# Kernel tuning notes

Measured on AMD Instinct MI355X. Metric: run time of the kernel, lower is better.

## Reference

```python
import jax, jax.numpy as jnp
import numpy as np

COST_CLASS, COST_BBOX, COST_GIOU = 1.0, 5.0, 2.0


def _lsa(cost):
    """Rectangular linear sum assignment (minimize), Jonker-Volgenant style.
    Returns (row_ind, col_ind) like scipy.optimize.linear_sum_assignment."""
    c = np.asarray(cost, dtype=np.float64)
    transposed = c.shape[0] > c.shape[1]
    if transposed:
        c = c.T
    n, m = c.shape  # n <= m
    INF = 1e18
    u = np.zeros(n + 1)
    v = np.zeros(m + 1)
    p = np.zeros(m + 1, dtype=np.int64)   # p[j]: row (1-based) matched to col j, 0 = free
    way = np.zeros(m + 1, dtype=np.int64)
    for i in range(1, n + 1):
        p[0] = i
        j0 = 0
        minv = np.full(m + 1, INF)
        used = np.zeros(m + 1, dtype=bool)
        while True:
            used[j0] = True
            i0 = p[j0]
            cur = c[i0 - 1, :] - u[i0] - v[1:]
            mv = minv[1:]
            upd = (~used[1:]) & (cur < mv)
            mv[upd] = cur[upd]
            way[1:][upd] = j0
            masked = np.where(used[1:], INF, mv)
            j1 = int(np.argmin(masked)) + 1
            delta = masked[j1 - 1]
            u[p[used]] += delta
            v[used] -= delta
            minv[1:][~used[1:]] -= delta
            j0 = j1
            if p[j0] == 0:
                break
        while j0:
            j1 = way[j0]
            p[j0] = p[j1]
            j0 = j1
    rows = p[1:] - 1
    cols = np.arange(m)
    keep = rows >= 0
    ri, ci = rows[keep], cols[keep]
    if transposed:
        ri, ci = ci, ri
    order = np.argsort(ri)
    return ri[order], ci[order]


def _solve_blocks(cost, n_per):
    """cost: np [Q, B*n_per]; solve LSA per diagonal block, return 0/1 solution."""
    Q, T = cost.shape
    B = T // n_per
    sol = np.zeros((Q, T), dtype=np.float32)
    for b in range(B):
        ri, ci = _lsa(cost[:, b * n_per:(b + 1) * n_per])
        sol[ri, b * n_per + ci] = 1.0
    return sol


def box_cxcywh_to_xyxy(b):
    cx, cy, w, h = jnp.split(b, 4, axis=-1)
    return jnp.concatenate([cx - 0.5 * w, cy - 0.5 * h, cx + 0.5 * w, cy + 0.5 * h], axis=-1)


def generalized_box_iou(b1, b2):
    # b1: [N,4] xyxy, b2: [M,4] xyxy -> [N,M]
    area1 = (b1[:, 2] - b1[:, 0]) * (b1[:, 3] - b1[:, 1])
    area2 = (b2[:, 2] - b2[:, 0]) * (b2[:, 3] - b2[:, 1])
    lt = jnp.maximum(b1[:, None, :2], b2[None, :, :2])
    rb = jnp.minimum(b1[:, None, 2:], b2[None, :, 2:])
    wh = jnp.clip(rb - lt, 0.0)
    inter = wh[..., 0] * wh[..., 1]
    union = area1[:, None] + area2[None, :] - inter
    iou = inter / union
    ltc = jnp.minimum(b1[:, None, :2], b2[None, :, :2])
    rbc = jnp.maximum(b1[:, None, 2:], b2[None, :, 2:])
    whc = jnp.clip(rbc - ltc, 0.0)
    areac = whc[..., 0] * whc[..., 1]
    return iou - (areac - union) / areac


def build_cost(pred_logits, pred_boxes, tgt_labels, tgt_boxes, n_per):
    B, Q, C = pred_logits.shape
    out_prob = jax.nn.softmax(pred_logits.reshape(B * Q, C), axis=-1)
    out_bbox = pred_boxes.reshape(B * Q, 4)
    cost_class = -out_prob[:, tgt_labels]                                  # [N,T]
    cost_bbox = jnp.sum(jnp.abs(out_bbox[:, None, :] - tgt_boxes[None, :, :]), axis=-1)  # L1 cdist
    cost_giou = -generalized_box_iou(box_cxcywh_to_xyxy(out_bbox), box_cxcywh_to_xyxy(tgt_boxes))
    cm = COST_BBOX * cost_bbox + COST_CLASS * cost_class + COST_GIOU * cost_giou
    cm = cm.reshape(B, Q, B, n_per)
    blocks = cm[jnp.arange(B), :, jnp.arange(B), :]        # diagonal blocks [B,Q,n_per]
    return jnp.transpose(blocks, (1, 0, 2)).reshape(Q, B * n_per)  # hstack -> [Q, T]


def setup_inputs() -> dict:
    key = jax.random.key(0)
    k1, k2, k3, k4 = jax.random.split(key, 4)
    B, Q, C, n_per = 16, 900, 92, 32
    T = B * n_per
    return {
        "pred_logits": jax.random.normal(k1, (B, Q, C), dtype=jnp.float32),
        "pred_boxes": jax.random.uniform(k2, (B, Q, 4), dtype=jnp.float32),
        "tgt_labels": jax.random.randint(k3, (T,), 0, C, dtype=jnp.int64),
        "tgt_boxes": jax.random.uniform(k4, (T, 4), dtype=jnp.float32),
        "n_targets": n_per,
    }


def reference(pred_logits, pred_boxes, tgt_labels, tgt_boxes, n_targets):
    n_per = int(n_targets)
    cost = build_cost(pred_logits, pred_boxes, tgt_labels, tgt_boxes, n_per)
    sol = jax.pure_callback(
        lambda c: _solve_blocks(np.asarray(c, dtype=np.float64), n_per),
        jax.ShapeDtypeStruct(cost.shape, jnp.float32),
        cost,
    )
    return sol
```

## Files before the change

kernel.cpp:

```cpp
#include <hip/hip_runtime.h>
#include <math.h>

#define BB 16
#define QQ 900
#define CC 92
#define NP 32
#define TT (BB*NP)
#define RSTRIDE 1024
#define NT 512

#define WSC_COST 0
#define WSC_MAX  (BB*NP*RSTRIDE*4)
#define WSC_SUM  (WSC_MAX + BB*QQ*4)
#define WSC_A    (WSC_SUM + BB*QQ*4)
#define WS_NEED  (WSC_A + TT*4)

__device__ __forceinline__ double mkdbl(int lo, int hi) {
    return __longlong_as_double(((long long)hi << 32) | (unsigned int)lo);
}
__device__ __forceinline__ double readlane_dbl(double x, int s) {
    long long l = __double_as_longlong(x);
    int lo = __builtin_amdgcn_readlane((int)l, s);
    int hi = __builtin_amdgcn_readlane((int)(l >> 32), s);
    return mkdbl(lo, hi);
}

#define DPP_MIN64(CTRL)                                                       \
    {                                                                         \
        long long _l = __double_as_longlong(m);                               \
        int _lo = (int)_l, _hi = (int)(_l >> 32);                             \
        int _olo = __builtin_amdgcn_update_dpp(_lo, _lo, CTRL, 0xf, 0xf, false); \
        int _ohi = __builtin_amdgcn_update_dpp(_hi, _hi, CTRL, 0xf, 0xf, false); \
        m = fmin(m, mkdbl(_olo, _ohi));                                       \
    }

__launch_bounds__(256)
__global__ void denom_kernel(const float* __restrict__ logits,
                             float* __restrict__ wmax,
                             float* __restrict__ wsum)
{
    int idx = blockIdx.x * 256 + threadIdx.x;
    if (idx >= BB * QQ) return;
    const float4* row4 = (const float4*)(logits + (size_t)idx * CC);
    float mx = -INFINITY;
    #pragma unroll
    for (int k = 0; k < 23; ++k) {
        float4 x = row4[k];
        mx = fmaxf(mx, x.x); mx = fmaxf(mx, x.y);
        mx = fmaxf(mx, x.z); mx = fmaxf(mx, x.w);
    }
    float s = 0.f;
    #pragma unroll
    for (int k = 0; k < 23; ++k) {
        float4 x = row4[k];
        s += expf(x.x - mx); s += expf(x.y - mx);
        s += expf(x.z - mx); s += expf(x.w - mx);
    }
    wmax[idx] = mx;
    wsum[idx] = s;
}

__launch_bounds__(256)
__global__ void cost_kernel(const float* __restrict__ logits,
                            const float* __restrict__ pboxes,
                            const int*   __restrict__ labels,
                            const float* __restrict__ tboxes,
                            const float* __restrict__ wmax,
                            const float* __restrict__ wsum,
                            float* __restrict__ wcost)
{
    const int r = blockIdx.x;
    const int b = r >> 5, t = r & 31;
    const float* lg = logits + (size_t)b * QQ * CC;
    const float* pb = pboxes + (size_t)b * QQ * 4;
    const float* tb = tboxes + (size_t)b * NP * 4;
    const float* smax = wmax + b * QQ;
    const float* ssum = wsum + b * QQ;

    const float t0 = tb[t*4+0], t1 = tb[t*4+1], t2 = tb[t*4+2], t3 = tb[t*4+3];
    const int   lt = labels[b * NP + t];
    const float tx1 = t0 - 0.5f*t2, ty1 = t1 - 0.5f*t3;
    const float tx2 = t0 + 0.5f*t2, ty2 = t1 + 0.5f*t3;
    const float area2 = (tx2-tx1)*(ty2-ty1);

    float* crow = wcost + (size_t)r * RSTRIDE;
    for (int q = threadIdx.x; q < RSTRIDE; q += 256) {
        float val = 0.f;
        if (q < QQ) {
            float l    = lg[q * CC + lt];
            float prob = expf(l - smax[q]) / ssum[q];
            float cclass = -prob;
            float p0 = pb[q*4+0], p1 = pb[q*4+1], p2 = pb[q*4+2], p3 = pb[q*4+3];
            float cbbox = fabsf(p0-t0) + fabsf(p1-t1)
                        + fabsf(p2-t2) + fabsf(p3-t3);
            float px1 = p0 - 0.5f*p2, py1 = p1 - 0.5f*p3;
            float px2 = p0 + 0.5f*p2, py2 = p1 + 0.5f*p3;
            float area1 = (px2-px1)*(py2-py1);
            float ltx = fmaxf(px1,tx1), lty = fmaxf(py1,ty1);
            float rbx = fminf(px2,tx2), rby = fminf(py2,ty2);
            float wx = fmaxf(rbx-ltx, 0.f), wy = fmaxf(rby-lty, 0.f);
            float inter = wx*wy;
            float uni = area1 + area2 - inter;
            float iou = inter / uni;
            float cx1 = fminf(px1,tx1), cy1 = fminf(py1,ty1);
            float cx2 = fmaxf(px2,tx2), cy2 = fmaxf(py2,ty2);
            float cwx = fmaxf(cx2-cx1, 0.f), cwy = fmaxf(cy2-cy1, 0.f);
            float areac = cwx*cwy;
            float giou = iou - (areac - uni) / areac;
            val = 5.f*cbbox + 1.f*cclass + 2.f*(-giou);
        }
        crow[q] = val;
    }
}

#define C_OFF_COST 0
#define C_SZ_COST  (NP * RSTRIDE * 4)
#define C_OFF_U    (C_OFF_COST + C_SZ_COST)
#define C_OFF_V    (C_OFF_U + 264)
#define C_OFF_FLAG (C_OFF_V + 7208)
#define C_DYN      (C_OFF_FLAG + 128)

__launch_bounds__(256)
__global__ void walk_kernel(const float* __restrict__ wcost,
                            int* __restrict__ wa)
{
    extern __shared__ char smem[];
    float*  s_cost = (float*)(smem + C_OFF_COST);
    double* s_u    = (double*)(smem + C_OFF_U);
    double* s_v    = (double*)(smem + C_OFF_V);
    volatile int* s_flag = (volatile int*)(smem + C_OFF_FLAG);

    const int b    = blockIdx.x;
    const int tid  = threadIdx.x;
    const int wv   = tid >> 6;
    const int lane = tid & 63;

    if (tid < 32) s_flag[tid] = 0;
    __syncthreads();

    if (wv != 0) {
        for (int t = wv - 1; t < NP; t += 3) {
            const float4* src =
                (const float4*)(wcost + ((size_t)(b * NP + t) * RSTRIDE));
            float4* dst = (float4*)(s_cost + t * RSTRIDE);
            float4 v0 = src[lane];
            float4 v1 = src[lane + 64];
            float4 v2 = src[lane + 128];
            float4 v3 = src[lane + 192];
            dst[lane]       = v0;
            dst[lane + 64]  = v1;
            dst[lane + 128] = v2;
            dst[lane + 192] = v3;
            asm volatile("s_waitcnt vmcnt(0) lgkmcnt(0)" ::: "memory");
            if (lane == 0) s_flag[t] = 1;
        }
        return;
    }

    for (int j = lane; j <= QQ; j += 64) s_v[j] = 0.0;
    if (lane <= NP) s_u[lane] = 0.0;
    asm volatile("s_waitcnt lgkmcnt(0)" ::: "memory");

    int acol = 0;
    const float4* cbase4 = (const float4*)s_cost;

    double vreg[16];
    #pragma unroll
    for (int k = 0; k < 16; ++k) {
        int col = 4 * lane + ((k >> 2) << 8) + (k & 3) + 1;
        vreg[k] = (col <= QQ) ? 0.0 : -1.0e300;
    }

    int nv = 0;

    while (nv < 1) {
        if (s_flag[0]) nv = 1;
        else __builtin_amdgcn_s_sleep(2);
    }
    float4 cf[4];
    {
        const float4* crow4 = cbase4;
        #pragma unroll
        for (int k = 0; k < 4; ++k) cf[k] = crow4[lane + (k << 6)];
    }

    for (int i = 1; i <= NP; ++i) {
        int i0 = i, j1prev = 0, T = 0;
        int path_reg = 1, row_reg = 1;

        for (int t = 1;; ++t) {
            if (lane == t) row_reg = i0;
            if (j1prev) {
                #pragma unroll
                for (int k = 0; k < 16; ++k) {
                    int col = 4 * lane + ((k >> 2) << 8) + (k & 3) + 1;
                    if (col == j1prev) vreg[k] = -1.0e300;
                }
            }

            double key[16];
            #pragma unroll
            for (int k = 0; k < 4; ++k) {
                const float* cp = (const float*)&cf[k];
                #pragma unroll
                for (int e2 = 0; e2 < 4; ++e2) {
                    int kk  = 4 * k + e2;
                    int col = 4 * lane + (k << 8) + e2 + 1;
                    double d = (double)cp[e2] - vreg[kk];
                    long long bits =
                        (__double_as_longlong(d) & ~2047LL) | (long long)col;
                    key[kk] = __longlong_as_double(bits);
                }
            }
            double a0 = fmin(key[0], key[1]),   a1 = fmin(key[2], key[3]);
            double a2 = fmin(key[4], key[5]),   a3 = fmin(key[6], key[7]);
            double a4 = fmin(key[8], key[9]),   a5 = fmin(key[10], key[11]);
            double a6 = fmin(key[12], key[13]), a7 = fmin(key[14], key[15]);
            double b0 = fmin(a0, a1), b1 = fmin(a2, a3);
            double b2 = fmin(a4, a5), b3 = fmin(a6, a7);
            double m  = fmin(fmin(b0, b1), fmin(b2, b3));

            DPP_MIN64(0x111);
            DPP_MIN64(0x112);
            DPP_MIN64(0x114);
            DPP_MIN64(0x118);
            DPP_MIN64(0x142);
            DPP_MIN64(0x143);

            int wlo = __builtin_amdgcn_readlane((int)__double_as_longlong(m), 63);
            int j1  = wlo & 2047;

            if (lane == t) path_reg = j1;

            unsigned long long mask = __ballot(acol == j1);
            if (mask == 0) { T = t; break; }
            int L = (int)__builtin_ctzll(mask);
            i0 = L + 1;
            j1prev = j1;

            const float4* crow4 = cbase4 + (size_t)L * (RSTRIDE / 4);
            #pragma unroll
            for (int k = 0; k < 4; ++k) cf[k] = crow4[lane + (k << 6)];
        }

        bool pre = false;
        if (i < NP) {
            if (nv > i) pre = true;
            else if (s_flag[29] && s_flag[30] && s_flag[31]) {
                nv = NP;
                pre = true;
            }
            if (pre) {
                const float4* crow4 = cbase4 + (size_t)i * (RSTRIDE / 4);
                #pragma unroll
                for (int k = 0; k < 4; ++k) cf[k] = crow4[lane + (k << 6)];
            }
        }

        const int  rt  = row_reg;
        const int  myj = path_reg;
        const bool act = (lane >= 1 && lane <= T);
        double mydelta = 0.0, uu = 0.0, vv = 0.0;
        if (act) {
            double cD = (double)s_cost[(rt - 1) * RSTRIDE + (myj - 1)];
            mydelta = (cD - s_u[rt]) - s_v[myj];
            uu = s_u[rt];
            vv = s_v[myj];
        }
        for (int s = 1; s <= T; ++s) {
            double ds = readlane_dbl(mydelta, s);
            int    js = __builtin_amdgcn_readlane(path_reg, s);
            int    rs = __builtin_amdgcn_readlane(row_reg, s);
            if (lane >= 1 && lane <= s) uu += ds;
            if (lane >= 1 && lane <  s) vv -= ds;
            if (rs == lane + 1) acol = js;
        }
        if (act) {
            s_u[rt]  = uu;
            s_v[myj] = vv;
        }
        for (int s = 1; s <= T; ++s) {
            int    js  = __builtin_amdgcn_readlane(path_reg, s);
            double vvs = readlane_dbl(vv, s);
            #pragma unroll
            for (int k = 0; k < 16; ++k) {
                int col = 4 * lane + ((k >> 2) << 8) + (k & 3) + 1;
                if (col == js) vreg[k] = vvs;
            }
        }

        if (i < NP && !pre) {
            while (nv <= i) {
                if (s_flag[nv]) ++nv;
                else __builtin_amdgcn_s_sleep(2);
            }
            const float4* crow4 = cbase4 + (size_t)i * (RSTRIDE / 4);
            #pragma unroll
            for (int k = 0; k < 4; ++k) cf[k] = crow4[lane + (k << 6)];
        }
    }

    if (lane < NP) wa[b * NP + lane] = acol - 1;
}

__launch_bounds__(256)
__global__ void epilogue_kernel(const int* __restrict__ wa,
                                float* __restrict__ out)
{
    int idx = blockIdx.x * 256 + threadIdx.x;
    if (idx >= QQ * BB * 8) return;
    int q   = idx >> 7;
    int rem = idx & 127;
    int b   = rem >> 3, f = rem & 7;
    int base = b * NP + 4 * f;
    int a0 = wa[base + 0], a1 = wa[base + 1];
    int a2 = wa[base + 2], a3 = wa[base + 3];
    float4 o;
    o.x = (a0 == q) ? 1.f : 0.f;
    o.y = (a1 == q) ? 1.f : 0.f;
    o.z = (a2 == q) ? 1.f : 0.f;
    o.w = (a3 == q) ? 1.f : 0.f;
    ((float4*)(out + (size_t)q * TT + b * NP))[f] = o;
}

#define OFF_COST 0
#define SZ_COST  (NP * RSTRIDE * 4)
#define OFF_U    (OFF_COST + SZ_COST)
#define OFF_V    (OFF_U + 264)
#define OFF_P    (OFF_V + 7208)
#define OFF_MAX  (OFF_P + 3604)
#define OFF_SUM  (OFF_MAX + 3600)
#define OFF_FLAG (OFF_SUM + 3600)
#define DYN_BYTES (OFF_FLAG + 128)

__launch_bounds__(NT)
__global__ void matcher_kernel(const float* __restrict__ logits,
                               const float* __restrict__ pboxes,
                               const int*   __restrict__ labels,
                               const float* __restrict__ tboxes,
                               float* __restrict__ out)
{
    extern __shared__ char smem[];
    float*  s_cost = (float*)(smem + OFF_COST);
    double* s_u    = (double*)(smem + OFF_U);
    double* s_v    = (double*)(smem + OFF_V);
    int*    s_p    = (int*)(smem + OFF_P);
    float*  s_max  = (float*)(smem + OFF_MAX);
    float*  s_sum  = (float*)(smem + OFF_SUM);
    volatile int* s_flag = (volatile int*)(smem + OFF_FLAG);

    const int b    = blockIdx.x;
    const int tid  = threadIdx.x;
    const int wv   = tid >> 6;
    const int lane = tid & 63;

    const float* lg = logits + (size_t)b * QQ * CC;
    if (tid < 32) s_flag[tid] = 0;
    for (int q = tid; q < QQ; q += NT) {
        const float4* row4 = (const float4*)(lg + q * CC);
        float mx = -INFINITY;
        #pragma unroll
        for (int k = 0; k < 23; ++k) {
            float4 x = row4[k];
            mx = fmaxf(mx, x.x); mx = fmaxf(mx, x.y);
            mx = fmaxf(mx, x.z); mx = fmaxf(mx, x.w);
        }
        float s = 0.f;
        #pragma unroll
        for (int k = 0; k < 23; ++k) {
            float4 x = row4[k];
            s += expf(x.x - mx); s += expf(x.y - mx);
            s += expf(x.z - mx); s += expf(x.w - mx);
        }
        s_max[q] = mx;
        s_sum[q] = s;
    }
    __syncthreads();

    const float* pb = pboxes + (size_t)b * QQ * 4;
    const float* tb = tboxes + (size_t)b * NP * 4;
    const int*   lb = labels + b * NP;

    if (wv != 0) {
        for (int t = wv - 1; t < NP; t += 7) {
            const float t0 = tb[t*4+0], t1 = tb[t*4+1],
                        t2 = tb[t*4+2], t3 = tb[t*4+3];
            const int   lt = lb[t];
            const float tx1 = t0 - 0.5f*t2, ty1 = t1 - 0.5f*t3;
            const float tx2 = t0 + 0.5f*t2, ty2 = t1 + 0.5f*t3;
            const float area2 = (tx2-tx1)*(ty2-ty1);
            #pragma unroll 4
            for (int it = 0; it < 16; ++it) {
                int q = (it << 6) + lane;
                float val = 0.f;
                if (q < QQ) {
                    float l    = lg[q * CC + lt];
                    float prob = expf(l - s_max[q]) / s_sum[q];
                    float cclass = -prob;
                    float p0 = pb[q*4+0], p1 = pb[q*4+1],
                          p2 = pb[q*4+2], p3 = pb[q*4+3];
                    float cbbox = fabsf(p0-t0) + fabsf(p1-t1)
                                + fabsf(p2-t2) + fabsf(p3-t3);
                    float px1 = p0 - 0.5f*p2, py1 = p1 - 0.5f*p3;
                    float px2 = p0 + 0.5f*p2, py2 = p1 + 0.5f*p3;
                    float area1 = (px2-px1)*(py2-py1);
                    float ltx = fmaxf(px1,tx1), lty = fmaxf(py1,ty1);
                    float rbx = fminf(px2,tx2), rby = fminf(py2,ty2);
                    float wx = fmaxf(rbx-ltx, 0.f), wy = fmaxf(rby-lty, 0.f);
                    float inter = wx*wy;
                    float uni = area1 + area2 - inter;
                    float iou = inter / uni;
                    float cx1 = fminf(px1,tx1), cy1 = fminf(py1,ty1);
                    float cx2 = fmaxf(px2,tx2), cy2 = fmaxf(py2,ty2);
                    float cwx = fmaxf(cx2-cx1, 0.f), cwy = fmaxf(cy2-cy1, 0.f);
                    float areac = cwx*cwy;
                    float giou = iou - (areac - uni) / areac;
                    val = 5.f*cbbox + 1.f*cclass + 2.f*(-giou);
                }
                s_cost[t * RSTRIDE + q] = val;
            }
            asm volatile("s_waitcnt lgkmcnt(0)" ::: "memory");
            if (lane == 0) s_flag[t] = 1;
        }
    } else {
        for (int j = lane; j <= QQ; j += 64) { s_p[j] = 0; s_v[j] = 0.0; }
        if (lane <= NP) s_u[lane] = 0.0;
        asm volatile("s_waitcnt lgkmcnt(0)" ::: "memory");

        int acol = 0;
        const float4* cbase4 = (const float4*)s_cost;

        double vreg[16];
        #pragma unroll
        for (int k = 0; k < 16; ++k) vreg[k] = 0.0;

        unsigned used0 = 0;
        #pragma unroll
        for (int k = 0; k < 16; ++k) {
            int col = 4 * lane + ((k >> 2) << 8) + (k & 3) + 1;
            if (col > QQ) used0 |= 1u << k;
        }

        int nv = 0;
        for (int i = 1; i <= NP; ++i) {
            while (nv < i) {
                if (s_flag[nv]) ++nv;
                else __builtin_amdgcn_s_sleep(2);
            }
            unsigned used = used0;
            int i0 = i, j1prev = 0, T = 0;
            int path_reg = 1, row_reg = 1;
            float4 cf[4];
            {
                const float4* crow4 = cbase4 + (size_t)(i0 - 1) * (RSTRIDE / 4);
                #pragma unroll
                for (int k = 0; k < 4; ++k) cf[k] = crow4[lane + (k << 6)];
            }
            for (int t = 1;; ++t) {
                if (lane == t) row_reg = i0;
                if (j1prev) {
                    int qp = j1prev - 1;
                    if (((qp >> 2) & 63) == lane)
                        used |= 1u << (((qp >> 8) << 2) | (qp & 3));
                }
                double key[16];
                #pragma unroll
                for (int k = 0; k < 4; ++k) {
                    const float* cp = (const float*)&cf[k];
                    #pragma unroll
                    for (int e2 = 0; e2 < 4; ++e2) {
                        int kk  = 4 * k + e2;
                        int col = 4 * lane + (k << 8) + e2 + 1;
                        double d = (double)cp[e2] - vreg[kk];
                        long long bits =
                            (__double_as_longlong(d) & ~2047LL) | (long long)col;
                        key[kk] = ((used >> kk) & 1u)
                                      ? 1e300 : __longlong_as_double(bits);
                    }
                }
                double a0 = fmin(key[0], key[1]),   a1 = fmin(key[2], key[3]);
                double a2 = fmin(key[4], key[5]),   a3 = fmin(key[6], key[7]);
                double a4 = fmin(key[8], key[9]),   a5 = fmin(key[10], key[11]);
                double a6 = fmin(key[12], key[13]), a7 = fmin(key[14], key[15]);
                double b0 = fmin(a0, a1), b1 = fmin(a2, a3);
                double b2 = fmin(a4, a5), b3 = fmin(a6, a7);
                double m  = fmin(fmin(b0, b1), fmin(b2, b3));
                DPP_MIN64(0x111); DPP_MIN64(0x112); DPP_MIN64(0x114);
                DPP_MIN64(0x118); DPP_MIN64(0x142); DPP_MIN64(0x143);
                int wlo = __builtin_amdgcn_readlane((int)__double_as_longlong(m), 63);
                int j1  = wlo & 2047;
                if (lane == t) path_reg = j1;
                unsigned long long mask = __ballot(acol == j1);
                if (mask == 0) { T = t; break; }
                int L = (int)__builtin_ctzll(mask);
                i0 = L + 1;
                j1prev = j1;
                const float4* crow4 = cbase4 + (size_t)L * (RSTRIDE / 4);
                #pragma unroll
                for (int k = 0; k < 4; ++k) cf[k] = crow4[lane + (k << 6)];
            }
            const int  rt  = row_reg;
            const int  myj = path_reg;
            const bool act = (lane >= 1 && lane <= T);
            double mydelta = 0.0, uu = 0.0, vv = 0.0;
            if (act) {
                double cD = (double)s_cost[(rt - 1) * RSTRIDE + (myj - 1)];
                mydelta = (cD - s_u[rt]) - s_v[myj];
                uu = s_u[rt];
                vv = s_v[myj];
            }
            for (int s = 1; s <= T; ++s) {
                double ds = readlane_dbl(mydelta, s);
                int    js = __builtin_amdgcn_readlane(path_reg, s);
                int    rs = __builtin_amdgcn_readlane(row_reg, s);
                if (lane >= 1 && lane <= s) uu += ds;
                if (lane >= 1 && lane <  s) vv -= ds;
                if (rs == lane + 1) acol = js;
            }
            if (act) {
                s_u[rt]  = uu;
                s_v[myj] = vv;
                s_p[myj] = rt;
            }
            for (int s = 1; s <= T; ++s) {
                int    js  = __builtin_amdgcn_readlane(path_reg, s);
                double vvs = readlane_dbl(vv, s);
                #pragma unroll
                for (int k = 0; k < 16; ++k) {
                    int col = 4 * lane + ((k >> 2) << 8) + (k & 3) + 1;
                    if (col == js) vreg[k] = vvs;
                }
            }
        }
    }
    __syncthreads();

    for (int e = tid; e < QQ * 8; e += NT) {
        int q = e >> 3;
        int f = e & 7;
        int pq = s_p[q + 1];
        int base = 4 * f;
        float4 o;
        o.x = (pq == base + 1) ? 1.f : 0.f;
        o.y = (pq == base + 2) ? 1.f : 0.f;
        o.z = (pq == base + 3) ? 1.f : 0.f;
        o.w = (pq == base + 4) ? 1.f : 0.f;
        ((float4*)(out + (size_t)q * TT + b * NP))[f] = o;
    }
}

extern "C" void kernel_launch(void* const* d_in, const int* in_sizes, int n_in,
                              void* d_out, int out_size, void* d_ws, size_t ws_size,
                              hipStream_t stream) {
    const float* logits = (const float*)d_in[0];
    const float* pboxes = (const float*)d_in[1];
    const int*   labels = (const int*)  d_in[2];
    const float* tboxes = (const float*)d_in[3];
    float* out = (float*)d_out;

    if (d_ws != nullptr && ws_size >= (size_t)WS_NEED) {
        float* wcost = (float*)((char*)d_ws + WSC_COST);
        float* wmax  = (float*)((char*)d_ws + WSC_MAX);
        float* wsum  = (float*)((char*)d_ws + WSC_SUM);
        int*   wa    = (int*)  ((char*)d_ws + WSC_A);

        (void)hipFuncSetAttribute((const void*)walk_kernel,
                                  hipFuncAttributeMaxDynamicSharedMemorySize,
                                  C_DYN);

        denom_kernel<<<(BB*QQ + 255)/256, 256, 0, stream>>>(logits, wmax, wsum);
        cost_kernel<<<BB*NP, 256, 0, stream>>>(logits, pboxes, labels, tboxes,
                                               wmax, wsum, wcost);
        walk_kernel<<<BB, 256, C_DYN, stream>>>(wcost, wa);
        epilogue_kernel<<<(QQ*BB*8 + 255)/256, 256, 0, stream>>>(wa, out);
    } else {
        (void)hipFuncSetAttribute((const void*)matcher_kernel,
                                  hipFuncAttributeMaxDynamicSharedMemorySize,
                                  DYN_BYTES);
        matcher_kernel<<<BB, NT, DYN_BYTES, stream>>>(logits, pboxes, labels,
                                                      tboxes, out);
    }
}
```

Before: 105.3 us.

## Fuse epilogue into walk kernel, keep row duals in registers, widen loader waves

```diff
diff --git a/kernel.cpp b/kernel.cpp
--- a/kernel.cpp
+++ b/kernel.cpp
@@ -22,6 +22,12 @@
     long long l = __double_as_longlong(x);
     int lo = __builtin_amdgcn_readlane((int)l, s);
     int hi = __builtin_amdgcn_readlane((int)(l >> 32), s);
+    return mkdbl(lo, hi);
+}
+__device__ __forceinline__ double bpermute_dbl(int srclane, double x) {
+    long long l = __double_as_longlong(x);
+    int lo = __builtin_amdgcn_ds_bpermute(srclane << 2, (int)l);
+    int hi = __builtin_amdgcn_ds_bpermute(srclane << 2, (int)(l >> 32));
     return mkdbl(lo, hi);
 }
 
@@ -115,20 +121,20 @@
 
 #define C_OFF_COST 0
 #define C_SZ_COST  (NP * RSTRIDE * 4)
-#define C_OFF_U    (C_OFF_COST + C_SZ_COST)
-#define C_OFF_V    (C_OFF_U + 264)
+#define C_OFF_V    (C_OFF_COST + C_SZ_COST)
 #define C_OFF_FLAG (C_OFF_V + 7208)
-#define C_DYN      (C_OFF_FLAG + 128)
-
-__launch_bounds__(256)
+#define C_OFF_ASN  (C_OFF_FLAG + 128)
+#define C_DYN      (C_OFF_ASN + 128)
+
+__launch_bounds__(512)
 __global__ void walk_kernel(const float* __restrict__ wcost,
-                            int* __restrict__ wa)
+                            float* __restrict__ out)
 {
     extern __shared__ char smem[];
     float*  s_cost = (float*)(smem + C_OFF_COST);
-    double* s_u    = (double*)(smem + C_OFF_U);
     double* s_v    = (double*)(smem + C_OFF_V);
     volatile int* s_flag = (volatile int*)(smem + C_OFF_FLAG);
+    int*    s_asn  = (int*)(smem + C_OFF_ASN);
 
     const int b    = blockIdx.x;
     const int tid  = threadIdx.x;
@@ -139,7 +145,7 @@
     __syncthreads();
 
     if (wv != 0) {
-        for (int t = wv - 1; t < NP; t += 3) {
+        for (int t = wv - 1; t < NP; t += 7) {
             const float4* src =
                 (const float4*)(wcost + ((size_t)(b * NP + t) * RSTRIDE));
             float4* dst = (float4*)(s_cost + t * RSTRIDE);
@@ -154,173 +160,175 @@
             asm volatile("s_waitcnt vmcnt(0) lgkmcnt(0)" ::: "memory");
             if (lane == 0) s_flag[t] = 1;
         }
-        return;
-    }
-
-    for (int j = lane; j <= QQ; j += 64) s_v[j] = 0.0;
-    if (lane <= NP) s_u[lane] = 0.0;
-    asm volatile("s_waitcnt lgkmcnt(0)" ::: "memory");
-
-    int acol = 0;
-    const float4* cbase4 = (const float4*)s_cost;
-
-    double vreg[16];
-    #pragma unroll
-    for (int k = 0; k < 16; ++k) {
-        int col = 4 * lane + ((k >> 2) << 8) + (k & 3) + 1;
-        vreg[k] = (col <= QQ) ? 0.0 : -1.0e300;
-    }
-
-    int nv = 0;
-
-    while (nv < 1) {
-        if (s_flag[0]) nv = 1;
-        else __builtin_amdgcn_s_sleep(2);
-    }
-    float4 cf[4];
-    {
-        const float4* crow4 = cbase4;
+    } else {
+        for (int j = lane; j <= QQ; j += 64) s_v[j] = 0.0;
+        asm volatile("s_waitcnt lgkmcnt(0)" ::: "memory");
+
+        int acol = 0;
+        double ureg = 0.0;
+        const float4* cbase4 = (const float4*)s_cost;
+
+        double vreg[16];
         #pragma unroll
-        for (int k = 0; k < 4; ++k) cf[k] = crow4[lane + (k << 6)];
-    }
-
-    for (int i = 1; i <= NP; ++i) {
-        int i0 = i, j1prev = 0, T = 0;
-        int path_reg = 1, row_reg = 1;
-
-        for (int t = 1;; ++t) {
-            if (lane == t) row_reg = i0;
-            if (j1prev) {
-                #pragma unroll
-                for (int k = 0; k < 16; ++k) {
-                    int col = 4 * lane + ((k >> 2) << 8) + (k & 3) + 1;
-                    if (col == j1prev) vreg[k] = -1.0e300;
-                }
-            }
-
-            double key[16];
-            #pragma unroll
-            for (int k = 0; k < 4; ++k) {
-                const float* cp = (const float*)&cf[k];
-                #pragma unroll
-                for (int e2 = 0; e2 < 4; ++e2) {
-                    int kk  = 4 * k + e2;
-                    int col = 4 * lane + (k << 8) + e2 + 1;
-                    double d = (double)cp[e2] - vreg[kk];
-                    long long bits =
-                        (__double_as_longlong(d) & ~2047LL) | (long long)col;
-                    key[kk] = __longlong_as_double(bits);
-                }
-            }
-            double a0 = fmin(key[0], key[1]),   a1 = fmin(key[2], key[3]);
-            double a2 = fmin(key[4], key[5]),   a3 = fmin(key[6], key[7]);
-            double a4 = fmin(key[8], key[9]),   a5 = fmin(key[10], key[11]);
-            double a6 = fmin(key[12], key[13]), a7 = fmin(key[14], key[15]);
-            double b0 = fmin(a0, a1), b1 = fmin(a2, a3);
-            double b2 = fmin(a4, a5), b3 = fmin(a6, a7);
-            double m  = fmin(fmin(b0, b1), fmin(b2, b3));
-
-            DPP_MIN64(0x111);
-            DPP_MIN64(0x112);
-            DPP_MIN64(0x114);
-            DPP_MIN64(0x118);
-            DPP_MIN64(0x142);
-            DPP_MIN64(0x143);
-
-            int wlo = __builtin_amdgcn_readlane((int)__double_as_longlong(m), 63);
-            int j1  = wlo & 2047;
-
-            if (lane == t) path_reg = j1;
-
-            unsigned long long mask = __ballot(acol == j1);
-            if (mask == 0) { T = t; break; }
-            int L = (int)__builtin_ctzll(mask);
-            i0 = L + 1;
-            j1prev = j1;
-
-            const float4* crow4 = cbase4 + (size_t)L * (RSTRIDE / 4);
+        for (int k = 0; k < 16; ++k) {
+            int col = 4 * lane + ((k >> 2) << 8) + (k & 3) + 1;
+            vreg[k] = (col <= QQ) ? 0.0 : -1.0e300;
+        }
+
+        int nv = 0;
+
+        while (nv < 1) {
+            if (s_flag[0]) nv = 1;
+            else __builtin_amdgcn_s_sleep(2);
+        }
+        float4 cf[4];
+        {
+            const float4* crow4 = cbase4;
             #pragma unroll
             for (int k = 0; k < 4; ++k) cf[k] = crow4[lane + (k << 6)];
         }
 
-        bool pre = false;
-        if (i < NP) {
-            if (nv > i) pre = true;
-            else if (s_flag[29] && s_flag[30] && s_flag[31]) {
-                nv = NP;
-                pre = true;
-            }
-            if (pre) {
+        for (int i = 1; i <= NP; ++i) {
+            int i0 = i, j1prev = 0, T = 0;
+            int path_reg = 1, row_reg = 1;
+
+            for (int t = 1;; ++t) {
+                if (lane == t) row_reg = i0;
+                if (j1prev) {
+                    #pragma unroll
+                    for (int k = 0; k < 16; ++k) {
+                        int col = 4 * lane + ((k >> 2) << 8) + (k & 3) + 1;
+                        if (col == j1prev) vreg[k] = -1.0e300;
+                    }
+                }
+
+                double key[16];
+                #pragma unroll
+                for (int k = 0; k < 4; ++k) {
+                    const float* cp = (const float*)&cf[k];
+                    #pragma unroll
+                    for (int e2 = 0; e2 < 4; ++e2) {
+                        int kk  = 4 * k + e2;
+                        int col = 4 * lane + (k << 8) + e2 + 1;
+                        double d = (double)cp[e2] - vreg[kk];
+                        long long bits =
+                            (__double_as_longlong(d) & ~2047LL) | (long long)col;
+                        key[kk] = __longlong_as_double(bits);
+                    }
+                }
+                double a0 = fmin(key[0], key[1]),   a1 = fmin(key[2], key[3]);
+                double a2 = fmin(key[4], key[5]),   a3 = fmin(key[6], key[7]);
+                double a4 = fmin(key[8], key[9]),   a5 = fmin(key[10], key[11]);
+                double a6 = fmin(key[12], key[13]), a7 = fmin(key[14], key[15]);
+                double b0 = fmin(a0, a1), b1 = fmin(a2, a3);
+                double b2 = fmin(a4, a5), b3 = fmin(a6, a7);
+                double m  = fmin(fmin(b0, b1), fmin(b2, b3));
+
+                DPP_MIN64(0x111);
+                DPP_MIN64(0x112);
+                DPP_MIN64(0x114);
+                DPP_MIN64(0x118);
+                DPP_MIN64(0x142);
+                DPP_MIN64(0x143);
+
+                int wlo = __builtin_amdgcn_readlane((int)__double_as_longlong(m), 63);
+                int j1  = wlo & 2047;
+
+                if (lane == t) path_reg = j1;
+
+                unsigned long long mask = __ballot(acol == j1);
+                if (mask == 0) { T = t; break; }
+                int L = (int)__builtin_ctzll(mask);
+                i0 = L + 1;
+                j1prev = j1;
+
+                const float4* crow4 = cbase4 + (size_t)L * (RSTRIDE / 4);
+                #pragma unroll
+                for (int k = 0; k < 4; ++k) cf[k] = crow4[lane + (k << 6)];
+            }
+
+            bool pre = false;
+            if (i < NP) {
+                if (nv > i) pre = true;
+                else if (s_flag[25] && s_flag[26] && s_flag[27] && s_flag[28]
+                      && s_flag[29] && s_flag[30] && s_flag[31]) {
+                    nv = NP;
+                    pre = true;
+                }
+                if (pre) {
+                    const float4* crow4 = cbase4 + (size_t)i * (RSTRIDE / 4);
+                    #pragma unroll
+                    for (int k = 0; k < 4; ++k) cf[k] = crow4[lane + (k << 6)];
+                }
+            }
+
+            const int  rt  = row_reg;
+            const int  myj = path_reg;
+            const bool act = (lane >= 1 && lane <= T);
+            double mydelta = 0.0, vv = 0.0;
+            {
+                double cD = 0.0, v0j = 0.0;
+                if (act) {
+                    cD  = (double)s_cost[(rt - 1) * RSTRIDE + (myj - 1)];
+                    v0j = s_v[myj];
+                }
+                double u0rt = bpermute_dbl(rt, ureg);
+                if (act) {
+                    mydelta = (cD - u0rt) - v0j;
+                    vv = v0j;
+                }
+            }
+            bool inpath = false;
+            for (int s = 1; s <= T; ++s) {
+                double ds = readlane_dbl(mydelta, s);
+                int    js = __builtin_amdgcn_readlane(path_reg, s);
+                int    rs = __builtin_amdgcn_readlane(row_reg, s);
+                if (lane + 1 == rs) inpath = true;
+                if (inpath) ureg += ds;
+                if (lane >= 1 && lane <  s) vv -= ds;
+                if (rs == lane + 1) acol = js;
+            }
+            if (T > 1) {
+                if (act) s_v[myj] = vv;
+                for (int s = 1; s <= T; ++s) {
+                    int    js  = __builtin_amdgcn_readlane(path_reg, s);
+                    double vvs = readlane_dbl(vv, s);
+                    #pragma unroll
+                    for (int k = 0; k < 16; ++k) {
+                        int col = 4 * lane + ((k >> 2) << 8) + (k & 3) + 1;
+                        if (col == js) vreg[k] = vvs;
+                    }
+                }
+            }
+
+            if (i < NP && !pre) {
+                while (nv <= i) {
+                    if (s_flag[nv]) ++nv;
+                    else __builtin_amdgcn_s_sleep(2);
+                }
                 const float4* crow4 = cbase4 + (size_t)i * (RSTRIDE / 4);
                 #pragma unroll
                 for (int k = 0; k < 4; ++k) cf[k] = crow4[lane + (k << 6)];
             }
         }
 
-        const int  rt  = row_reg;
-        const int  myj = path_reg;
-        const bool act = (lane >= 1 && lane <= T);
-        double mydelta = 0.0, uu = 0.0, vv = 0.0;
-        if (act) {
-            double cD = (double)s_cost[(rt - 1) * RSTRIDE + (myj - 1)];
-            mydelta = (cD - s_u[rt]) - s_v[myj];
-            uu = s_u[rt];
-            vv = s_v[myj];
-        }
-        for (int s = 1; s <= T; ++s) {
-            double ds = readlane_dbl(mydelta, s);
-            int    js = __builtin_amdgcn_readlane(path_reg, s);
-            int    rs = __builtin_amdgcn_readlane(row_reg, s);
-            if (lane >= 1 && lane <= s) uu += ds;
-            if (lane >= 1 && lane <  s) vv -= ds;
-            if (rs == lane + 1) acol = js;
-        }
-        if (act) {
-            s_u[rt]  = uu;
-            s_v[myj] = vv;
-        }
-        for (int s = 1; s <= T; ++s) {
-            int    js  = __builtin_amdgcn_readlane(path_reg, s);
-            double vvs = readlane_dbl(vv, s);
-            #pragma unroll
-            for (int k = 0; k < 16; ++k) {
-                int col = 4 * lane + ((k >> 2) << 8) + (k & 3) + 1;
-                if (col == js) vreg[k] = vvs;
-            }
-        }
-
-        if (i < NP && !pre) {
-            while (nv <= i) {
-                if (s_flag[nv]) ++nv;
-                else __builtin_amdgcn_s_sleep(2);
-            }
-            const float4* crow4 = cbase4 + (size_t)i * (RSTRIDE / 4);
-            #pragma unroll
-            for (int k = 0; k < 4; ++k) cf[k] = crow4[lane + (k << 6)];
-        }
-    }
-
-    if (lane < NP) wa[b * NP + lane] = acol - 1;
-}
-
-__launch_bounds__(256)
-__global__ void epilogue_kernel(const int* __restrict__ wa,
-                                float* __restrict__ out)
-{
-    int idx = blockIdx.x * 256 + threadIdx.x;
-    if (idx >= QQ * BB * 8) return;
-    int q   = idx >> 7;
-    int rem = idx & 127;
-    int b   = rem >> 3, f = rem & 7;
-    int base = b * NP + 4 * f;
-    int a0 = wa[base + 0], a1 = wa[base + 1];
-    int a2 = wa[base + 2], a3 = wa[base + 3];
-    float4 o;
-    o.x = (a0 == q) ? 1.f : 0.f;
-    o.y = (a1 == q) ? 1.f : 0.f;
-    o.z = (a2 == q) ? 1.f : 0.f;
-    o.w = (a3 == q) ? 1.f : 0.f;
-    ((float4*)(out + (size_t)q * TT + b * NP))[f] = o;
+        if (lane < NP) s_asn[lane] = acol - 1;
+    }
+    __syncthreads();
+
+    for (int e = tid; e < QQ * 8; e += 512) {
+        int q = e >> 3;
+        int f = e & 7;
+        int base = 4 * f;
+        int a0 = s_asn[base + 0], a1 = s_asn[base + 1];
+        int a2 = s_asn[base + 2], a3 = s_asn[base + 3];
+        float4 o;
+        o.x = (a0 == q) ? 1.f : 0.f;
+        o.y = (a1 == q) ? 1.f : 0.f;
+        o.z = (a2 == q) ? 1.f : 0.f;
+        o.w = (a3 == q) ? 1.f : 0.f;
+        ((float4*)(out + (size_t)q * TT + b * NP))[f] = o;
+    }
 }
 
 #define OFF_COST 0
@@ -562,7 +570,6 @@
         float* wcost = (float*)((char*)d_ws + WSC_COST);
         float* wmax  = (float*)((char*)d_ws + WSC_MAX);
         float* wsum  = (float*)((char*)d_ws + WSC_SUM);
-        int*   wa    = (int*)  ((char*)d_ws + WSC_A);
 
         (void)hipFuncSetAttribute((const void*)walk_kernel,
                                   hipFuncAttributeMaxDynamicSharedMemorySize,
@@ -571,8 +578,7 @@
         denom_kernel<<<(BB*QQ + 255)/256, 256, 0, stream>>>(logits, wmax, wsum);
         cost_kernel<<<BB*NP, 256, 0, stream>>>(logits, pboxes, labels, tboxes,
                                                wmax, wsum, wcost);
-        walk_kernel<<<BB, 256, C_DYN, stream>>>(wcost, wa);
-        epilogue_kernel<<<(QQ*BB*8 + 255)/256, 256, 0, stream>>>(wa, out);
+        walk_kernel<<<BB, 512, C_DYN, stream>>>(wcost, out);
     } else {
         (void)hipFuncSetAttribute((const void*)matcher_kernel,
                                   hipFuncAttributeMaxDynamicSharedMemorySize,
```

Result: faster. 98.96 us, median of 2 (-6.0%).
